# Kernel tuning notes

Hardware: AMD Instinct MI355X
Metric: run time of the kernel (lower is better)

Reference implementation:

```python
import jax, jax.numpy as jnp
import numpy as np

B, P, Q, H = 8, 2048, 512, 1024


def setup_inputs() -> dict:
    key = jax.random.key(0)
    k1, k2, k3, k4, k5 = jax.random.split(key, 5)
    passage = jax.random.normal(k1, (B, P, H), dtype=jnp.float32)
    question = jax.random.normal(k2, (B, Q, H), dtype=jnp.float32)
    q_mask = jax.random.randint(k3, (B, Q), 0, 2, dtype=jnp.int32)
    # map_linear params (torch Linear: y = x @ W.T + b)
    bound = 1.0 / np.sqrt(H)
    map_W = jax.random.uniform(k4, (H, H), jnp.float32, -bound, bound)
    map_b = jax.random.uniform(k5, (H,), jnp.float32, -bound, bound)
    return {"passage": passage, "question": question, "q_mask": q_mask,
            "map_W": map_W, "map_b": map_b}


def reference(passage, question, q_mask, map_W, map_b):
    # scores: [B, P, Q]
    scores = jnp.einsum("bph,bqh->bpq", passage, question)
    mask = q_mask.astype(scores.dtype)[:, None, :]  # [B, 1, Q], broadcasts over P
    # multiplicative masked softmax + renormalize (memory_efficient=False path)
    a = jax.nn.softmax(scores * mask, axis=-1) * mask
    alpha = a / (jnp.sum(a, axis=-1, keepdims=True) + 1e-13)
    # attend: [B, P, H]
    out = jnp.einsum("bpq,bqh->bph", alpha, question)
    # fused linear + ReLU
    return jax.nn.relu(jnp.einsum("bph,oh->bpo", out, map_W) + map_b)
```

## Files before the change

kernel.cpp:

```cpp
#include <hip/hip_runtime.h>
#include <hip/hip_bf16.h>

typedef _Float16 f16;
typedef _Float16 f16x8 __attribute__((ext_vector_type(8)));
typedef _Float16 f16x4 __attribute__((ext_vector_type(4)));
typedef float f32x4 __attribute__((ext_vector_type(4)));
typedef int i32x4 __attribute__((ext_vector_type(4)));

#define B_ 8
#define P_ 2048
#define Q_ 512
#define H_ 1024

__device__ __forceinline__ void gload_lds16(const void* g, void* l) {
  __builtin_amdgcn_global_load_lds(
      (const __attribute__((address_space(1))) void*)g,
      (__attribute__((address_space(3))) void*)l, 16, 0, 0);
}

__global__ __launch_bounds__(256) void k_cvt16(const float* __restrict__ x,
                                               f16* __restrict__ y, int n4) {
  int i = blockIdx.x * blockDim.x + threadIdx.x;
  int stride = gridDim.x * blockDim.x;
  for (; i < n4; i += stride) {
    f32x4 v = ((const f32x4*)x)[i];
    f16x4 h;
#pragma unroll
    for (int j = 0; j < 4; ++j) h[j] = (f16)v[j];
    ((f16x4*)y)[i] = h;
  }
}

__global__ __launch_bounds__(256) void k_transpose(const float* __restrict__ q,
                                                   f16* __restrict__ qT,
                                                   f16* __restrict__ q16) {
  __shared__ float t[64][65];
  int b = blockIdx.z;
  int h0 = blockIdx.x * 64, q0 = blockIdx.y * 64;
  int tid = threadIdx.x;
  int c4 = (tid & 15) * 4;
  int r16 = tid >> 4;
  const float* src = q + ((long)b * Q_ + q0) * H_ + h0;
  f16* d16 = q16 + ((long)b * Q_ + q0) * H_ + h0;
#pragma unroll
  for (int i = 0; i < 4; ++i) {
    int r = r16 + i * 16;
    f32x4 v = *(const f32x4*)(src + (long)r * H_ + c4);
    f16x4 s;
#pragma unroll
    for (int j = 0; j < 4; ++j) s[j] = (f16)v[j];
    *(f16x4*)(d16 + (long)r * H_ + c4) = s;
    t[c4 + 0][r] = v[0];
    t[c4 + 1][r] = v[1];
    t[c4 + 2][r] = v[2];
    t[c4 + 3][r] = v[3];
  }
  __syncthreads();
  f16* dst = qT + ((long)b * H_ + h0) * Q_ + q0;
#pragma unroll
  for (int i = 0; i < 4; ++i) {
    int hr = r16 + i * 16;
    f16x4 o;
#pragma unroll
    for (int j = 0; j < 4; ++j) o[j] = (f16)t[hr][c4 + j];
    *(f16x4*)(dst + (long)hr * Q_ + c4) = o;
  }
}

__global__ __launch_bounds__(512, 2) void k_gemm1(
    const float* __restrict__ passage, const f16* __restrict__ q16,
    float* __restrict__ S) {
  constexpr int NT = H_ / 32;
  __shared__ __align__(16) f16 smem[40960];

  int orig = blockIdx.x;
  int wg = (orig & 7) * 32 + (orig >> 3);
  int bx = wg & 1, by = (wg >> 1) & 15, z = wg >> 5;
  int row0 = by * 128, col0 = bx * 256;

  int tid = threadIdx.x, wv = tid >> 6, lane = tid & 63;
  int fr = lane & 15, kq = lane >> 4;
  int wr = (wv >> 2) * 64, wc = (wv & 3) * 64;
  int swz = (kq ^ ((fr >> 1) & 3)) * 8;

  int ar = tid >> 2, ac = tid & 3;
  const float* gA = passage + ((long)(z * P_ + row0 + ar)) * H_ + ac * 8;
  int aw = ar * 32 + ((ac ^ ((ar >> 1) & 3)) * 8);

  const f16* gB = q16 + ((long)(z * Q_ + col0 + (tid >> 2))) * H_ +
                  (((tid & 3) ^ ((tid >> 3) & 3)) * 8);

  auto stageB = [&](int t) {
    const f16* g = gB + t * 32;
    f16* l = smem + 8192 + (t & 3) * 8192 + wv * 512;
    gload_lds16(g, l);
    gload_lds16(g + (long)128 * H_, l + 4096);
  };
  auto writeA = [&](int t, f32x4 lo, f32x4 hi) {
    f16x8 h;
#pragma unroll
    for (int j = 0; j < 4; ++j) {
      h[j] = (f16)lo[j];
      h[4 + j] = (f16)hi[j];
    }
    *(f16x8*)(smem + (t & 1) * 4096 + aw) = h;
  };

  f32x4 acc[4][4] = {};
  f32x4 a0lo, a0hi, a1lo, a1hi;

  a0lo = *(const f32x4*)(gA);
  a0hi = *(const f32x4*)(gA + 4);
  a1lo = *(const f32x4*)(gA + 32);
  a1hi = *(const f32x4*)(gA + 36);
  stageB(0);
  stageB(1);
  stageB(2);
  writeA(0, a0lo, a0hi);
  asm volatile("s_waitcnt vmcnt(4) lgkmcnt(0)" ::: "memory");
  __builtin_amdgcn_s_barrier();
  __builtin_amdgcn_sched_barrier(0);

#pragma unroll 4
  for (int t = 0; t < NT; ++t) {
    if (t + 2 < NT) {
      const float* g = gA + (t + 2) * 32;
      if (t & 1) {
        a1lo = *(const f32x4*)(g);
        a1hi = *(const f32x4*)(g + 4);
      } else {
        a0lo = *(const f32x4*)(g);
        a0hi = *(const f32x4*)(g + 4);
      }
    }
    if (t + 3 < NT) stageB(t + 3);
    f16x8 af[4], bf[4];
    const f16* Ab = smem + (t & 1) * 4096;
    const f16* Bb = smem + 8192 + (t & 3) * 8192;
#pragma unroll
    for (int m = 0; m < 4; ++m)
      af[m] = *(const f16x8*)(Ab + (wr + m * 16 + fr) * 32 + swz);
#pragma unroll
    for (int n = 0; n < 4; ++n)
      bf[n] = *(const f16x8*)(Bb + (wc + n * 16 + fr) * 32 + swz);
    if (t + 1 < NT)
      writeA(t + 1, (t & 1) ? a0lo : a1lo, (t & 1) ? a0hi : a1hi);
    __builtin_amdgcn_s_setprio(1);
#pragma unroll
    for (int m = 0; m < 4; ++m)
#pragma unroll
      for (int n = 0; n < 4; ++n)
        acc[m][n] = __builtin_amdgcn_mfma_f32_16x16x32_f16(af[m], bf[n],
                                                           acc[m][n], 0, 0, 0);
    __builtin_amdgcn_s_setprio(0);
    if (t <= NT - 4)
      asm volatile("s_waitcnt vmcnt(6) lgkmcnt(0)" ::: "memory");
    else if (t == NT - 3)
      asm volatile("s_waitcnt vmcnt(4) lgkmcnt(0)" ::: "memory");
    else
      asm volatile("s_waitcnt vmcnt(0) lgkmcnt(0)" ::: "memory");
    if (t < NT - 1) {
      __builtin_amdgcn_s_barrier();
      __builtin_amdgcn_sched_barrier(0);
    }
  }

  float* Sp = S + (long)z * P_ * Q_;
  int r0 = row0 + wr + (lane >> 4) * 4;
  int c0 = col0 + wc + fr;
#pragma unroll
  for (int m = 0; m < 4; ++m)
#pragma unroll
    for (int n = 0; n < 4; ++n)
#pragma unroll
      for (int j = 0; j < 4; ++j)
        Sp[(long)(r0 + m * 16 + j) * Q_ + c0 + n * 16] = acc[m][n][j];
}

__global__ __launch_bounds__(256) void k_softmax(const float* __restrict__ S,
                                                 const int* __restrict__ qmask,
                                                 f16* __restrict__ alpha) {
  int row = blockIdx.x * 4 + (threadIdx.x >> 6);
  int lane = threadIdx.x & 63;
  int b = row >> 11;
  const float* s = S + (long)row * Q_;
  const int* mp = qmask + b * Q_;
  f32x4 v0 = ((const f32x4*)s)[lane * 2];
  f32x4 v1 = ((const f32x4*)s)[lane * 2 + 1];
  i32x4 m0 = ((const i32x4*)mp)[lane * 2];
  i32x4 m1 = ((const i32x4*)mp)[lane * 2 + 1];
  float t[8], mf[8];
#pragma unroll
  for (int j = 0; j < 4; ++j) {
    mf[j] = (float)m0[j];     t[j] = v0[j] * mf[j];
    mf[4 + j] = (float)m1[j]; t[4 + j] = v1[j] * mf[4 + j];
  }
  float mx = t[0];
#pragma unroll
  for (int j = 1; j < 8; ++j) mx = fmaxf(mx, t[j]);
  for (int o = 32; o; o >>= 1) mx = fmaxf(mx, __shfl_xor(mx, o, 64));
  float e[8], Z = 0.f, Sm = 0.f;
#pragma unroll
  for (int j = 0; j < 8; ++j) {
    e[j] = expf(t[j] - mx);
    Z += e[j];
    Sm += e[j] * mf[j];
  }
  for (int o = 32; o; o >>= 1) {
    Z += __shfl_xor(Z, o, 64);
    Sm += __shfl_xor(Sm, o, 64);
  }
  float inv = 1.0f / (Sm + 1e-13f * Z);
  f16x8 out;
#pragma unroll
  for (int j = 0; j < 8; ++j) out[j] = (f16)(e[j] * mf[j] * inv);
  *(f16x8*)(alpha + (long)row * Q_ + lane * 8) = out;
}

template <int EPI, int NT>
__global__ __launch_bounds__(512, 2) void k_gemm256(
    const f16* __restrict__ A, const f16* __restrict__ Bm,
    void* __restrict__ Cv, const float* __restrict__ bias, int N, int gx,
    int gy, long sA, long sB, long sC) {
  constexpr int K = NT * 32;
  __shared__ __align__(16) f16 smem[65536];

  int nwg = gridDim.x;
  int orig = blockIdx.x;
  int wg = (orig & 7) * (nwg >> 3) + (orig >> 3);
  int bx = wg % gx;
  int tt = wg / gx;
  int by = tt % gy;
  int z = tt / gy;
  int row0 = by * 256, col0 = bx * 256;
  A += z * sA;
  Bm += z * sB;

  int tid = threadIdx.x, wv = tid >> 6, lane = tid & 63;

  bool isA = wv < 4;
  int u0 = (wv & 3) * 4;
  int srow = u0 * 16 + (lane >> 2);
  int sclog = ((lane & 3) ^ ((lane >> 3) & 3)) * 8;
  const f16* sbaseG = isA ? A + (long)(row0 + srow) * K + sclog
                          : Bm + (long)(col0 + srow) * K + sclog;
  int sbaseL = (isA ? 0 : 8192) + u0 * 512;

  auto stage = [&](int tile) {
    const f16* g = sbaseG + (long)tile * 32;
    f16* l = smem + (tile & 3) * 16384 + sbaseL;
#pragma unroll
    for (int j = 0; j < 4; ++j) gload_lds16(g + (long)j * 16 * K, l + j * 512);
  };

  int wr = (wv >> 2) * 128, wc = (wv & 3) * 64;
  int fr = lane & 15, kq = lane >> 4;
  int swz = (kq ^ ((fr >> 1) & 3)) * 8 + fr * 32;

  f32x4 acc[8][4] = {};
  auto compute = [&](int t) {
    const f16* bufA = smem + (t & 3) * 16384;
    const f16* bufB = bufA + 8192;
    f16x8 af[8], bfr[4];
#pragma unroll
    for (int m = 0; m < 8; ++m)
      af[m] = *(const f16x8*)(bufA + (wr + m * 16) * 32 + swz);
#pragma unroll
    for (int n = 0; n < 4; ++n)
      bfr[n] = *(const f16x8*)(bufB + (wc + n * 16) * 32 + swz);
#pragma unroll
    for (int m = 0; m < 8; ++m)
#pragma unroll
      for (int n = 0; n < 4; ++n)
        acc[m][n] = __builtin_amdgcn_mfma_f32_16x16x32_f16(af[m], bfr[n],
                                                           acc[m][n], 0, 0, 0);
  };

  stage(0);
  stage(1);
  stage(2);
  asm volatile("s_waitcnt vmcnt(8)" ::: "memory");
  __builtin_amdgcn_s_barrier();
  __builtin_amdgcn_sched_barrier(0);
  for (int t = 0; t < NT - 3; ++t) {
    stage(t + 3);
    compute(t);
    asm volatile("s_waitcnt vmcnt(8)" ::: "memory");
    __builtin_amdgcn_s_barrier();
    __builtin_amdgcn_sched_barrier(0);
  }
  compute(NT - 3);
  asm volatile("s_waitcnt vmcnt(4)" ::: "memory");
  __builtin_amdgcn_s_barrier();
  __builtin_amdgcn_sched_barrier(0);
  compute(NT - 2);
  asm volatile("s_waitcnt vmcnt(0)" ::: "memory");
  __builtin_amdgcn_s_barrier();
  __builtin_amdgcn_sched_barrier(0);
  compute(NT - 1);

  int r0 = row0 + wr + (lane >> 4) * 4;
  int c0 = col0 + wc + fr;
  if constexpr (EPI == 1) {
    f16* C = (f16*)Cv + z * sC;
#pragma unroll
    for (int m = 0; m < 8; ++m)
#pragma unroll
      for (int n = 0; n < 4; ++n)
#pragma unroll
        for (int j = 0; j < 4; ++j)
          C[(long)(r0 + m * 16 + j) * N + c0 + n * 16] = (f16)acc[m][n][j];
  } else {
    float* C = (float*)Cv;
#pragma unroll
    for (int n = 0; n < 4; ++n) {
      float bv = bias[c0 + n * 16];
#pragma unroll
      for (int m = 0; m < 8; ++m)
#pragma unroll
        for (int j = 0; j < 4; ++j) {
          float v = acc[m][n][j] + bv;
          C[(long)(r0 + m * 16 + j) * N + c0 + n * 16] = fmaxf(v, 0.f);
        }
    }
  }
}

extern "C" void kernel_launch(void* const* d_in, const int* in_sizes, int n_in,
                              void* d_out, int out_size, void* d_ws,
                              size_t ws_size, hipStream_t stream) {
  const float* passage = (const float*)d_in[0];
  const float* question = (const float*)d_in[1];
  const int* qmask = (const int*)d_in[2];
  const float* mapW = (const float*)d_in[3];
  const float* mapb = (const float*)d_in[4];

  char* ws = (char*)d_ws;
  size_t off = 0;
  auto alloc = [&](size_t bytes) {
    void* p = ws + off;
    off += (bytes + 255) & ~(size_t)255;
    return p;
  };
  f16* q16 = (f16*)alloc((size_t)B_ * Q_ * H_ * 2);
  f16* qT = (f16*)alloc((size_t)B_ * H_ * Q_ * 2);
  f16* w16 = (f16*)alloc((size_t)H_ * H_ * 2);
  f16* alpha = (f16*)alloc((size_t)B_ * P_ * Q_ * 2);
  f16* O = (f16*)alloc((size_t)B_ * P_ * H_ * 2);
  float* S = (float*)alloc((size_t)B_ * P_ * Q_ * 4);

  k_cvt16<<<512, 256, 0, stream>>>(mapW, w16, H_ * H_ / 4);
  k_transpose<<<dim3(H_ / 64, Q_ / 64, B_), 256, 0, stream>>>(question, qT,
                                                              q16);

  k_gemm1<<<256, 512, 0, stream>>>(passage, q16, S);

  k_softmax<<<B_ * P_ / 4, 256, 0, stream>>>(S, qmask, alpha);

  k_gemm256<1, Q_ / 32><<<256, 512, 0, stream>>>(
      alpha, qT, O, nullptr, H_, H_ / 256, P_ / 256, (long)P_ * Q_,
      (long)H_ * Q_, (long)P_ * H_);

  k_gemm256<2, H_ / 32><<<256, 512, 0, stream>>>(
      O, w16, d_out, mapb, H_, H_ / 256, (B_ * P_) / 256, 0, 0, 0);
}
```

Before: 123.5 us.

## Pre-convert passage to fp16 and stream both GEMM1 operands via async LDS loads

Adds a separate conversion kernel that turns the fp32 passage into fp16, reusing the O buffer, so GEMM1 can load both A and B tiles with global_load_lds into a unified 4-slot ring. This removes the register-staged fp32 loads, in-kernel conversion and explicit LDS writes from the GEMM main loop and simplifies the wait/barrier schedule. The cost is an extra kernel pass that reads 64MB of fp32 and writes 32MB of fp16, plus GEMM1 re-reading the fp16 copy.

```diff
diff --git a/kernel.cpp b/kernel.cpp
--- a/kernel.cpp
+++ b/kernel.cpp
@@ -68,10 +68,11 @@
 }
 
 __global__ __launch_bounds__(512, 2) void k_gemm1(
-    const float* __restrict__ passage, const f16* __restrict__ q16,
+    const f16* __restrict__ p16, const f16* __restrict__ q16,
     float* __restrict__ S) {
   constexpr int NT = H_ / 32;
-  __shared__ __align__(16) f16 smem[40960];
+  constexpr int SLOT = 12288;
+  __shared__ __align__(16) f16 smem[4 * SLOT];
 
   int orig = blockIdx.x;
   int wg = (orig & 7) * 32 + (orig >> 3);
@@ -80,90 +81,64 @@
 
   int tid = threadIdx.x, wv = tid >> 6, lane = tid & 63;
   int fr = lane & 15, kq = lane >> 4;
+
+  int scl = ((tid & 3) ^ ((tid >> 3) & 3)) * 8;
+  int R0 = tid >> 2;
+  const f16* g0 = p16 + (long)(z * P_ + row0 + R0) * H_ + scl;
+  const f16* g1 = q16 + (long)(z * Q_ + col0 + R0) * H_ + scl;
+  const f16* g2 = g1 + (long)128 * H_;
+
+  auto stage = [&](int t) {
+    f16* l = smem + (t & 3) * SLOT + wv * 512;
+    gload_lds16(g0 + t * 32, l);
+    gload_lds16(g1 + t * 32, l + 4096);
+    gload_lds16(g2 + t * 32, l + 8192);
+  };
+
   int wr = (wv >> 2) * 64, wc = (wv & 3) * 64;
-  int swz = (kq ^ ((fr >> 1) & 3)) * 8;
-
-  int ar = tid >> 2, ac = tid & 3;
-  const float* gA = passage + ((long)(z * P_ + row0 + ar)) * H_ + ac * 8;
-  int aw = ar * 32 + ((ac ^ ((ar >> 1) & 3)) * 8);
-
-  const f16* gB = q16 + ((long)(z * Q_ + col0 + (tid >> 2))) * H_ +
-                  (((tid & 3) ^ ((tid >> 3) & 3)) * 8);
-
-  auto stageB = [&](int t) {
-    const f16* g = gB + t * 32;
-    f16* l = smem + 8192 + (t & 3) * 8192 + wv * 512;
-    gload_lds16(g, l);
-    gload_lds16(g + (long)128 * H_, l + 4096);
-  };
-  auto writeA = [&](int t, f32x4 lo, f32x4 hi) {
-    f16x8 h;
-#pragma unroll
-    for (int j = 0; j < 4; ++j) {
-      h[j] = (f16)lo[j];
-      h[4 + j] = (f16)hi[j];
-    }
-    *(f16x8*)(smem + (t & 1) * 4096 + aw) = h;
-  };
+  int swz = (kq ^ ((fr >> 1) & 3)) * 8 + fr * 32;
 
   f32x4 acc[4][4] = {};
-  f32x4 a0lo, a0hi, a1lo, a1hi;
-
-  a0lo = *(const f32x4*)(gA);
-  a0hi = *(const f32x4*)(gA + 4);
-  a1lo = *(const f32x4*)(gA + 32);
-  a1hi = *(const f32x4*)(gA + 36);
-  stageB(0);
-  stageB(1);
-  stageB(2);
-  writeA(0, a0lo, a0hi);
-  asm volatile("s_waitcnt vmcnt(4) lgkmcnt(0)" ::: "memory");
-  __builtin_amdgcn_s_barrier();
-  __builtin_amdgcn_sched_barrier(0);
-
-#pragma unroll 4
-  for (int t = 0; t < NT; ++t) {
-    if (t + 2 < NT) {
-      const float* g = gA + (t + 2) * 32;
-      if (t & 1) {
-        a1lo = *(const f32x4*)(g);
-        a1hi = *(const f32x4*)(g + 4);
-      } else {
-        a0lo = *(const f32x4*)(g);
-        a0hi = *(const f32x4*)(g + 4);
-      }
-    }
-    if (t + 3 < NT) stageB(t + 3);
-    f16x8 af[4], bf[4];
-    const f16* Ab = smem + (t & 1) * 4096;
-    const f16* Bb = smem + 8192 + (t & 3) * 8192;
+  auto compute = [&](int t) {
+    const f16* bufA = smem + (t & 3) * SLOT;
+    const f16* bufB = bufA + 4096;
+    f16x8 af[4], bfr[4];
 #pragma unroll
     for (int m = 0; m < 4; ++m)
-      af[m] = *(const f16x8*)(Ab + (wr + m * 16 + fr) * 32 + swz);
+      af[m] = *(const f16x8*)(bufA + (wr + m * 16) * 32 + swz);
 #pragma unroll
     for (int n = 0; n < 4; ++n)
-      bf[n] = *(const f16x8*)(Bb + (wc + n * 16 + fr) * 32 + swz);
-    if (t + 1 < NT)
-      writeA(t + 1, (t & 1) ? a0lo : a1lo, (t & 1) ? a0hi : a1hi);
-    __builtin_amdgcn_s_setprio(1);
+      bfr[n] = *(const f16x8*)(bufB + (wc + n * 16) * 32 + swz);
 #pragma unroll
     for (int m = 0; m < 4; ++m)
 #pragma unroll
       for (int n = 0; n < 4; ++n)
-        acc[m][n] = __builtin_amdgcn_mfma_f32_16x16x32_f16(af[m], bf[n],
+        acc[m][n] = __builtin_amdgcn_mfma_f32_16x16x32_f16(af[m], bfr[n],
                                                            acc[m][n], 0, 0, 0);
-    __builtin_amdgcn_s_setprio(0);
-    if (t <= NT - 4)
-      asm volatile("s_waitcnt vmcnt(6) lgkmcnt(0)" ::: "memory");
-    else if (t == NT - 3)
-      asm volatile("s_waitcnt vmcnt(4) lgkmcnt(0)" ::: "memory");
-    else
-      asm volatile("s_waitcnt vmcnt(0) lgkmcnt(0)" ::: "memory");
-    if (t < NT - 1) {
-      __builtin_amdgcn_s_barrier();
-      __builtin_amdgcn_sched_barrier(0);
-    }
-  }
+  };
+
+  stage(0);
+  stage(1);
+  stage(2);
+  asm volatile("s_waitcnt vmcnt(6)" ::: "memory");
+  __builtin_amdgcn_s_barrier();
+  __builtin_amdgcn_sched_barrier(0);
+  for (int t = 0; t < NT - 3; ++t) {
+    stage(t + 3);
+    compute(t);
+    asm volatile("s_waitcnt vmcnt(6)" ::: "memory");
+    __builtin_amdgcn_s_barrier();
+    __builtin_amdgcn_sched_barrier(0);
+  }
+  compute(NT - 3);
+  asm volatile("s_waitcnt vmcnt(3)" ::: "memory");
+  __builtin_amdgcn_s_barrier();
+  __builtin_amdgcn_sched_barrier(0);
+  compute(NT - 2);
+  asm volatile("s_waitcnt vmcnt(0)" ::: "memory");
+  __builtin_amdgcn_s_barrier();
+  __builtin_amdgcn_sched_barrier(0);
+  compute(NT - 1);
 
   float* Sp = S + (long)z * P_ * Q_;
   int r0 = row0 + wr + (lane >> 4) * 4;
@@ -346,14 +321,16 @@
   f16* qT = (f16*)alloc((size_t)B_ * H_ * Q_ * 2);
   f16* w16 = (f16*)alloc((size_t)H_ * H_ * 2);
   f16* alpha = (f16*)alloc((size_t)B_ * P_ * Q_ * 2);
-  f16* O = (f16*)alloc((size_t)B_ * P_ * H_ * 2);
+  f16* p16 = (f16*)alloc((size_t)B_ * P_ * H_ * 2);
   float* S = (float*)alloc((size_t)B_ * P_ * Q_ * 4);
+  f16* O = p16;
 
   k_cvt16<<<512, 256, 0, stream>>>(mapW, w16, H_ * H_ / 4);
+  k_cvt16<<<2048, 256, 0, stream>>>(passage, p16, B_ * P_ * H_ / 4);
   k_transpose<<<dim3(H_ / 64, Q_ / 64, B_), 256, 0, stream>>>(question, qT,
                                                               q16);
 
-  k_gemm1<<<256, 512, 0, stream>>>(passage, q16, S);
+  k_gemm1<<<256, 512, 0, stream>>>(p16, q16, S);
 
   k_softmax<<<B_ * P_ / 4, 256, 0, stream>>>(S, qmask, alpha);
 
```

Result: no change. 124.4 us (+0.8%).
